# Kernel optimization log

Hardware: AMD Instinct MI355X
Metric: run time of the kernel (lower is better)

The kernel has to match this reference:

```python
import jax, jax.numpy as jnp
import numpy as np

B, F, E = 1024, 1024, 256      # batch, flat_shape (mobilenet), embedding_size
L1, L2, L3 = 16, 8, 32         # level1 classes, level2 classes per branch, level3 classes per leaf
NE3 = L1 * L2                  # 128 leaf (level-3) classifier heads


def setup_inputs() -> dict:
    key = jax.random.key(0)
    ks = jax.random.split(key, 10)
    w = lambda k, shape: (jax.random.normal(k, shape, jnp.float32) * 0.02)
    return {
        "features_x": jax.random.normal(ks[0], (B, F), jnp.float32),
        "features_y": jax.random.normal(ks[1], (B, F), jnp.float32),
        # level-1 head: Linear(F->E, no bias) + LayerNorm + ReLU + Linear(E->L1)
        "l1_W1": w(ks[2], (F, E)),
        "l1_g": jnp.ones((E,), jnp.float32), "l1_b": jnp.zeros((E,), jnp.float32),
        "l1_W2": w(ks[3], (E, L1)), "l1_b2": jnp.zeros((L1,), jnp.float32),
        # level-2 heads (one per level-1 class), stacked on a leading expert axis
        "l2_W1": w(ks[4], (L1, F, E)),
        "l2_g": jnp.ones((L1, E), jnp.float32), "l2_b": jnp.zeros((L1, E), jnp.float32),
        "l2_W2": w(ks[5], (L1, E, L2)), "l2_b2": jnp.zeros((L1, L2), jnp.float32),
        # level-3 heads (flattened [level1][level2] -> NE3 experts)
        "l3_W1": w(ks[6], (NE3, F, E)),
        "l3_g": jnp.ones((NE3, E), jnp.float32), "l3_b": jnp.zeros((NE3, E), jnp.float32),
        "l3_W2": w(ks[7], (NE3, E, L3)), "l3_b2": jnp.zeros((NE3, L3), jnp.float32),
    }


def _ln(h, g, b, eps=1e-5):
    m = jnp.mean(h, axis=-1, keepdims=True)
    v = jnp.mean(jnp.square(h - m), axis=-1, keepdims=True)
    return (h - m) * jax.lax.rsqrt(v + eps) * g + b


def reference(features_x, features_y,
              l1_W1, l1_g, l1_b, l1_W2, l1_b2,
              l2_W1, l2_g, l2_b, l2_W2, l2_b2,
              l3_W1, l3_g, l3_b, l3_W2, l3_b2):
    # Dropout is identity in eval mode.
    x, y = features_x, features_y
    rows = jnp.arange(x.shape[0])

    # level 1: single head on x
    h1 = jax.nn.relu(_ln(x @ l1_W1, l1_g, l1_b))
    logits1 = h1 @ l1_W2 + l1_b2                                # [B, L1]
    idx1 = jnp.argmax(logits1, axis=-1)                         # argmax(softmax) == argmax

    # level 2: routed head on 0.6*x + 0.4*y; compute all L1 heads batched, gather selected
    ft = 0.6 * x + 0.4 * y
    h2 = jax.nn.relu(_ln(jnp.einsum('bf,efh->beh', ft, l2_W1), l2_g, l2_b))  # [B, L1, E]
    logits2_all = jnp.einsum('beh,ehc->bec', h2, l2_W2) + l2_b2              # [B, L1, L2]
    logits2 = logits2_all[rows, idx1]                                        # [B, L2]
    idx2 = jnp.argmax(logits2, axis=-1)

    # level 3: doubly-routed head on x; flat expert index = idx1*L2 + idx2
    eidx = idx1 * logits2.shape[-1] + idx2
    h3 = jax.nn.relu(_ln(jnp.einsum('bf,efh->beh', x, l3_W1), l3_g, l3_b))   # [B, NE3, E]
    logits3_all = jnp.einsum('beh,ehc->bec', h3, l3_W2) + l3_b2              # [B, NE3, L3]
    logits3 = logits3_all[rows, eidx]                                        # [B, L3]

    # uniform class counts => pad_sequence is a no-op
    return (logits1, logits2, logits3)
```

## Files before the change

### kernel.cpp

```cpp
#include <hip/hip_runtime.h>


#define B_    1024
#define F_    1024
#define E_    256
#define NL1   16
#define NL2   8
#define NL3   32
#define NE3_  128
#define CS1   4
#define CS2   8
#define CS3   16
#define MAXCH2 160
#define MAXCH3 192
#define OUT2_OFF (B_ * NL1)
#define OUT3_OFF (B_ * (NL1 + NL2))

typedef __attribute__((ext_vector_type(8))) short bf16x8_t;
typedef __attribute__((ext_vector_type(4))) float f32x4_t;

__device__ __forceinline__ float b2f(unsigned short u) {
    union { unsigned int i; float f; } v; v.i = ((unsigned int)u) << 16; return v.f;
}
__device__ __forceinline__ unsigned short f2b(float f) {
    union { float f; unsigned int i; } v; v.f = f;
    unsigned int x = v.i; x += 0x7fffu + ((x >> 16) & 1u);
    return (unsigned short)(x >> 16);
}

template<int R, int NC>
__device__ void head_chunk(
    const float* __restrict__ in,
    const void* W1v, const void* gv_, const void* bv_,
    const void* W2v, const void* b2v, int bf,
    float* part, float* hn, float* red, float* lg, int t)
{
    const int lane = t & 63;
    const int grp  = t >> 6;
    const int e0   = lane * 4;

    float acc[R][4];
    #pragma unroll
    for (int r = 0; r < R; ++r) { acc[r][0]=0.f; acc[r][1]=0.f; acc[r][2]=0.f; acc[r][3]=0.f; }

    const float* ing = in + grp * 256;

    if (bf) {
        const unsigned short* W = (const unsigned short*)W1v + (size_t)grp * 256 * E_;
        for (int f0 = 0; f0 < 256; f0 += 16) {
            ushort4 w[16];
            #pragma unroll
            for (int k = 0; k < 16; ++k)
                w[k] = *(const ushort4*)(W + (size_t)(f0 + k) * E_ + e0);
            #pragma unroll
            for (int q = 0; q < 4; ++q) {
                float4 xq[R];
                #pragma unroll
                for (int r = 0; r < R; ++r)
                    xq[r] = *(const float4*)(ing + r * F_ + f0 + q * 4);
                #pragma unroll
                for (int k2 = 0; k2 < 4; ++k2) {
                    ushort4 ww = w[q * 4 + k2];
                    float w0 = b2f(ww.x), w1 = b2f(ww.y), w2 = b2f(ww.z), w3 = b2f(ww.w);
                    #pragma unroll
                    for (int r = 0; r < R; ++r) {
                        float xv = (k2 == 0) ? xq[r].x : (k2 == 1) ? xq[r].y
                                 : (k2 == 2) ? xq[r].z : xq[r].w;
                        acc[r][0] += xv * w0; acc[r][1] += xv * w1;
                        acc[r][2] += xv * w2; acc[r][3] += xv * w3;
                    }
                }
            }
        }
    } else {
        const float* W = (const float*)W1v + (size_t)grp * 256 * E_;
        for (int f0 = 0; f0 < 256; f0 += 8) {
            float4 w[8];
            #pragma unroll
            for (int k = 0; k < 8; ++k)
                w[k] = *(const float4*)(W + (size_t)(f0 + k) * E_ + e0);
            #pragma unroll
            for (int q = 0; q < 2; ++q) {
                float4 xq[R];
                #pragma unroll
                for (int r = 0; r < R; ++r)
                    xq[r] = *(const float4*)(ing + r * F_ + f0 + q * 4);
                #pragma unroll
                for (int k2 = 0; k2 < 4; ++k2) {
                    float4 ww = w[q * 4 + k2];
                    #pragma unroll
                    for (int r = 0; r < R; ++r) {
                        float xv = (k2 == 0) ? xq[r].x : (k2 == 1) ? xq[r].y
                                 : (k2 == 2) ? xq[r].z : xq[r].w;
                        acc[r][0] += xv * ww.x; acc[r][1] += xv * ww.y;
                        acc[r][2] += xv * ww.z; acc[r][3] += xv * ww.w;
                    }
                }
            }
        }
    }

    #pragma unroll
    for (int r = 0; r < R; ++r) {
        part[(size_t)(grp * R + r) * E_ + e0 + 0] = acc[r][0];
        part[(size_t)(grp * R + r) * E_ + e0 + 1] = acc[r][1];
        part[(size_t)(grp * R + r) * E_ + e0 + 2] = acc[r][2];
        part[(size_t)(grp * R + r) * E_ + e0 + 3] = acc[r][3];
    }
    __syncthreads();

    float h[R];
    #pragma unroll
    for (int r = 0; r < R; ++r)
        h[r] = part[(0 * R + r) * E_ + t] + part[(1 * R + r) * E_ + t]
             + part[(2 * R + r) * E_ + t] + part[(3 * R + r) * E_ + t];

    #pragma unroll
    for (int r = 0; r < R; ++r) {
        float s = h[r], ss = h[r] * h[r];
        #pragma unroll
        for (int o = 32; o > 0; o >>= 1) { s += __shfl_xor(s, o); ss += __shfl_xor(ss, o); }
        if (lane == 0) { red[(grp * R + r) * 2 + 0] = s; red[(grp * R + r) * 2 + 1] = ss; }
    }
    __syncthreads();

    float gv, bv;
    if (bf) { gv = b2f(((const unsigned short*)gv_)[t]); bv = b2f(((const unsigned short*)bv_)[t]); }
    else    { gv = ((const float*)gv_)[t];               bv = ((const float*)bv_)[t]; }

    #pragma unroll
    for (int r = 0; r < R; ++r) {
        float S  = red[(0*R+r)*2] + red[(1*R+r)*2] + red[(2*R+r)*2] + red[(3*R+r)*2];
        float SS = red[(0*R+r)*2+1] + red[(1*R+r)*2+1] + red[(2*R+r)*2+1] + red[(3*R+r)*2+1];
        float m    = S * (1.0f / E_);
        float var  = SS * (1.0f / E_) - m * m;
        float rstd = rsqrtf(var + 1e-5f);
        hn[r * E_ + t] = fmaxf((h[r] - m) * rstd * gv + bv, 0.0f);
    }
    __syncthreads();

    constexpr int RN = R * NC;
    constexpr int G  = 256 / RN;
    constexpr int CH = E_ / G;
    const int oi = t % RN, j = t / RN, r = oi / NC, c = oi % NC;
    float a = 0.f;
    if (bf) {
        const unsigned short* W = (const unsigned short*)W2v;
        #pragma unroll 8
        for (int e = j * CH; e < j * CH + CH; ++e) a += hn[r * E_ + e] * b2f(W[(size_t)e * NC + c]);
    } else {
        const float* W = (const float*)W2v;
        #pragma unroll 8
        for (int e = j * CH; e < j * CH + CH; ++e) a += hn[r * E_ + e] * W[(size_t)e * NC + c];
    }
    float bias = bf ? b2f(((const unsigned short*)b2v)[c]) : ((const float*)b2v)[c];
    if (G > 1) {
        part[t] = a;
        __syncthreads();
        if (j == 0) {
            float sum = a;
            #pragma unroll
            for (int jj = 1; jj < G; ++jj) sum += part[jj * RN + oi];
            lg[oi] = sum + bias;
        }
    } else {
        lg[oi] = a + bias;
    }
    __syncthreads();
}

__global__ void dtype_sniff_kernel(const unsigned int* l1g_words, int* flag) {
    if (threadIdx.x == 0 && blockIdx.x == 0)
        *flag = (l1g_words[0] == 0x3F803F80u) ? 1 : 0;
}

__global__ __launch_bounds__(256) void mlc_level1_kernel(
    const void* x, const void* W1, const void* g, const void* b,
    const void* W2, const void* b2, void* out, int* idx1, const int* flagp)
{
    __shared__ float in_s[CS1 * F_];
    __shared__ float part[4 * CS1 * E_];
    __shared__ float hn[CS1 * E_];
    __shared__ float red[4 * CS1 * 2];
    __shared__ float lg[CS1 * NL1];

    const int t = threadIdx.x;
    const int bf = *flagp;
    const int row0 = blockIdx.x * CS1;

    #pragma unroll
    for (int r = 0; r < CS1; ++r) {
        if (bf) {
            ushort4 xv = ((const ushort4*)x)[(size_t)(row0 + r) * 256 + t];
            in_s[r * F_ + t*4+0] = b2f(xv.x); in_s[r * F_ + t*4+1] = b2f(xv.y);
            in_s[r * F_ + t*4+2] = b2f(xv.z); in_s[r * F_ + t*4+3] = b2f(xv.w);
        } else {
            float4 xv = ((const float4*)x)[(size_t)(row0 + r) * 256 + t];
            in_s[r * F_ + t*4+0] = xv.x; in_s[r * F_ + t*4+1] = xv.y;
            in_s[r * F_ + t*4+2] = xv.z; in_s[r * F_ + t*4+3] = xv.w;
        }
    }
    __syncthreads();

    head_chunk<CS1, NL1>(in_s, W1, g, b, W2, b2, bf, part, hn, red, lg, t);

    if (t < CS1 * NL1) {
        int r = t / NL1, c = t % NL1;
        size_t o = (size_t)(row0 + r) * NL1 + c;
        if (bf) ((unsigned short*)out)[o] = f2b(lg[t]);
        else    ((float*)out)[o] = lg[t];
        if (c == 0) {
            float best = lg[r * NL1]; int bi = 0;
            #pragma unroll
            for (int cc = 1; cc < NL1; ++cc)
                if (lg[r * NL1 + cc] > best) { best = lg[r * NL1 + cc]; bi = cc; }
            idx1[row0 + r] = bi;
        }
    }
}

template<int NEXP, int MAXCH, int CHUNK>
__global__ __launch_bounds__(1024) void mlc_route_kernel(
    const int* __restrict__ src, int* __restrict__ rows_out, int4* __restrict__ chunks_out)
{
    __shared__ int hist[NEXP], offs[NEXP], cur[NEXP];
    const int t = threadIdx.x;
    if (t < NEXP) hist[t] = 0;
    __syncthreads();
    int e = src[t];
    if (e < 0) e = 0; if (e >= NEXP) e = NEXP - 1;
    atomicAdd(&hist[e], 1);
    __syncthreads();
    if (t == 0) {
        int o = 0;
        for (int i = 0; i < NEXP; ++i) { offs[i] = o; cur[i] = o; o += hist[i]; }
    }
    __syncthreads();
    int pos = atomicAdd(&cur[e], 1);
    if (pos >= 0 && pos < B_) rows_out[pos] = t;
    if (t == 0) {
        int nch = 0;
        for (int i = 0; i < NEXP; ++i) {
            int n = hist[i], st = offs[i];
            for (int j = 0; j < n && nch < MAXCH; j += CHUNK)
                chunks_out[nch++] = make_int4(i, st + j, min(CHUNK, n - j), 0);
        }
        for (; nch < MAXCH; ++nch) chunks_out[nch] = make_int4(0, 0, 0, 0);
    }
}

__global__ __launch_bounds__(256) void mlc_level2_kernel(
    const void* x, const void* y,
    const void* W1b, const void* gb, const void* bb,
    const void* W2b, const void* b2b,
    const int4* __restrict__ chunks, const int* __restrict__ rowlist,
    void* out, int* eidx, const int* flagp)
{
    __shared__ float in_s[CS2 * F_];
    __shared__ float part[4 * CS2 * E_];
    __shared__ float hn[CS2 * E_];
    __shared__ float red[4 * CS2 * 2];
    __shared__ float lg[CS2 * NL2];
    __shared__ int4  chs;
    __shared__ int   rows_s[CS2];

    const int t = threadIdx.x;
    const int bf = *flagp;

    if (t == 0) chs = chunks[blockIdx.x];
    __syncthreads();
    const int expert = chs.x, start = chs.y, count = chs.z;
    if (count <= 0) return;
    if (t < CS2) rows_s[t] = (t < count) ? rowlist[start + t] : -1;
    __syncthreads();

    #pragma unroll
    for (int r = 0; r < CS2; ++r) {
        int row = rows_s[r];
        float f0 = 0.f, f1 = 0.f, f2 = 0.f, f3 = 0.f;
        if (row >= 0) {
            if (bf) {
                ushort4 xv = ((const ushort4*)x)[(size_t)row * 256 + t];
                ushort4 yv = ((const ushort4*)y)[(size_t)row * 256 + t];
                f0 = 0.6f * b2f(xv.x) + 0.4f * b2f(yv.x);
                f1 = 0.6f * b2f(xv.y) + 0.4f * b2f(yv.y);
                f2 = 0.6f * b2f(xv.z) + 0.4f * b2f(yv.z);
                f3 = 0.6f * b2f(xv.w) + 0.4f * b2f(yv.w);
            } else {
                float4 xv = ((const float4*)x)[(size_t)row * 256 + t];
                float4 yv = ((const float4*)y)[(size_t)row * 256 + t];
                f0 = 0.6f * xv.x + 0.4f * yv.x; f1 = 0.6f * xv.y + 0.4f * yv.y;
                f2 = 0.6f * xv.z + 0.4f * yv.z; f3 = 0.6f * xv.w + 0.4f * yv.w;
            }
        }
        in_s[r * F_ + t*4+0] = f0; in_s[r * F_ + t*4+1] = f1;
        in_s[r * F_ + t*4+2] = f2; in_s[r * F_ + t*4+3] = f3;
    }
    __syncthreads();

    const void* W1 = bf ? (const void*)((const unsigned short*)W1b + (size_t)expert * F_ * E_)
                        : (const void*)((const float*)W1b + (size_t)expert * F_ * E_);
    const void* g  = bf ? (const void*)((const unsigned short*)gb + (size_t)expert * E_)
                        : (const void*)((const float*)gb + (size_t)expert * E_);
    const void* b  = bf ? (const void*)((const unsigned short*)bb + (size_t)expert * E_)
                        : (const void*)((const float*)bb + (size_t)expert * E_);
    const void* W2 = bf ? (const void*)((const unsigned short*)W2b + (size_t)expert * E_ * NL2)
                        : (const void*)((const float*)W2b + (size_t)expert * E_ * NL2);
    const void* b2 = bf ? (const void*)((const unsigned short*)b2b + (size_t)expert * NL2)
                        : (const void*)((const float*)b2b + (size_t)expert * NL2);

    head_chunk<CS2, NL2>(in_s, W1, g, b, W2, b2, bf, part, hn, red, lg, t);

    if (t < CS2 * NL2) {
        int r = t / NL2, c = t % NL2;
        if (r < count) {
            size_t o = (size_t)OUT2_OFF + (size_t)rows_s[r] * NL2 + c;
            if (bf) ((unsigned short*)out)[o] = f2b(lg[t]);
            else    ((float*)out)[o] = lg[t];
            if (c == 0) {
                float best = lg[r * NL2]; int bi = 0;
                #pragma unroll
                for (int cc = 1; cc < NL2; ++cc)
                    if (lg[r * NL2 + cc] > best) { best = lg[r * NL2 + cc]; bi = cc; }
                eidx[rows_s[r]] = expert * NL2 + bi;
            }
        }
    }
}


__device__ __forceinline__ void stage_rows(
    unsigned short* xs, const void* xg, const int* rows, int bf, int t)
{
    const int r = t >> 4;
    const int row = rows[r];
    #pragma unroll
    for (int i = 0; i < 8; ++i) {
        const int c  = (t & 15) + 16 * i;
        const int cs = c ^ (r & 7);
        uint4 v = make_uint4(0u, 0u, 0u, 0u);
        if (row >= 0) {
            if (bf) {
                v = *(const uint4*)((const unsigned short*)xg + (size_t)row * F_ + c * 8);
            } else {
                const float* xf = (const float*)xg + (size_t)row * F_ + c * 8;
                float4 fa = *(const float4*)xf;
                float4 fb = *(const float4*)(xf + 4);
                v.x = ((unsigned)f2b(fa.y) << 16) | f2b(fa.x);
                v.y = ((unsigned)f2b(fa.w) << 16) | f2b(fa.z);
                v.z = ((unsigned)f2b(fb.y) << 16) | f2b(fb.x);
                v.w = ((unsigned)f2b(fb.w) << 16) | f2b(fb.z);
            }
        }
        *(uint4*)(xs + (size_t)r * F_ + cs * 8) = v;
    }
}

__device__ void mfma_w1s(const unsigned short* xs, const void* W1v, int bf,
                         float* h, int t)
{
    const int l    = t & 63;
    const int w    = t >> 6;
    const int u    = l >> 4;
    const int row  = l & 15;
    const int colb = w * 64 + row;

    f32x4_t acc[4];
    #pragma unroll
    for (int tl = 0; tl < 4; ++tl) acc[tl] = (f32x4_t){0.f, 0.f, 0.f, 0.f};

    if (bf) {
        const unsigned short* __restrict__ W = (const unsigned short*)W1v;
        for (int k0 = 0; k0 < F_; k0 += 32) {
            const int cs = ((k0 >> 3) + u) ^ (row & 7);
            bf16x8_t ax = *(const bf16x8_t*)(xs + (size_t)row * F_ + cs * 8);
            const unsigned short* __restrict__ Wk = W + (size_t)(k0 + u * 8) * E_ + colb;
            #pragma unroll
            for (int tl = 0; tl < 4; ++tl) {
                bf16x8_t b;
                #pragma unroll
                for (int e = 0; e < 8; ++e) b[e] = (short)Wk[e * E_ + tl * 16];
                acc[tl] = __builtin_amdgcn_mfma_f32_16x16x32_bf16(ax, b, acc[tl], 0, 0, 0);
            }
        }
    } else {
        const float* __restrict__ W = (const float*)W1v;
        for (int k0 = 0; k0 < F_; k0 += 32) {
            const int cs = ((k0 >> 3) + u) ^ (row & 7);
            bf16x8_t ax = *(const bf16x8_t*)(xs + (size_t)row * F_ + cs * 8);
            const float* __restrict__ Wk = W + (size_t)(k0 + u * 8) * E_ + colb;
            #pragma unroll
            for (int tl = 0; tl < 4; ++tl) {
                bf16x8_t b;
                #pragma unroll
                for (int e = 0; e < 8; ++e) b[e] = (short)f2b(Wk[e * E_ + tl * 16]);
                acc[tl] = __builtin_amdgcn_mfma_f32_16x16x32_bf16(ax, b, acc[tl], 0, 0, 0);
            }
        }
    }

    #pragma unroll
    for (int tl = 0; tl < 4; ++tl) {
        #pragma unroll
        for (int j = 0; j < 4; ++j)
            h[(size_t)(u * 4 + j) * E_ + colb + tl * 16] = acc[tl][j];
    }
}

__device__ void ln_relu16(float* h, const void* g_, const void* b_,
                          int bf, int t, float* red)
{
    __syncthreads();
    const int l = t & 63, w = t >> 6;
    float hv[16];
    #pragma unroll
    for (int r = 0; r < 16; ++r) hv[r] = h[(size_t)r * E_ + t];

    #pragma unroll
    for (int r = 0; r < 16; ++r) {
        float s = hv[r], ss = hv[r] * hv[r];
        #pragma unroll
        for (int o = 32; o > 0; o >>= 1) { s += __shfl_xor(s, o); ss += __shfl_xor(ss, o); }
        if (l == 0) { red[(w * 16 + r) * 2] = s; red[(w * 16 + r) * 2 + 1] = ss; }
    }
    __syncthreads();

    float gv, bv;
    if (bf) { gv = b2f(((const unsigned short*)g_)[t]); bv = b2f(((const unsigned short*)b_)[t]); }
    else    { gv = ((const float*)g_)[t];               bv = ((const float*)b_)[t]; }

    #pragma unroll
    for (int r = 0; r < 16; ++r) {
        float S  = red[r * 2]     + red[(16 + r) * 2]     + red[(32 + r) * 2]     + red[(48 + r) * 2];
        float SS = red[r * 2 + 1] + red[(16 + r) * 2 + 1] + red[(32 + r) * 2 + 1] + red[(48 + r) * 2 + 1];
        float m    = S * (1.0f / E_);
        float var  = SS * (1.0f / E_) - m * m;
        float rstd = rsqrtf(var + 1e-5f);
        h[(size_t)r * E_ + t] = fmaxf((hv[r] - m) * rstd * gv + bv, 0.0f);
    }
    __syncthreads();
}

__global__ __launch_bounds__(256) void MultiLevelClassifier_26491358282059_kernel(
    const void* x,
    const void* W1b, const void* gb, const void* bb,
    const void* W2b, const void* b2b,
    const int4* __restrict__ chunks, const int* __restrict__ rowlist,
    void* out, const int* flagp)
{
    __shared__ __align__(16) unsigned short xs[16 * F_];
    __shared__ float h[16 * E_];
    __shared__ float red[128];
    __shared__ int4  chs;
    __shared__ int   rows_s[16];

    const int t  = threadIdx.x;
    const int bf = *flagp;

    if (t == 0) chs = chunks[blockIdx.x];
    __syncthreads();
    const int expert = chs.x, start = chs.y, count = chs.z;
    if (count <= 0) return;
    if (t < 16) rows_s[t] = (t < count) ? rowlist[start + t] : -1;
    __syncthreads();

    stage_rows(xs, x, rows_s, bf, t);
    __syncthreads();

    const void* W1 = bf ? (const void*)((const unsigned short*)W1b + (size_t)expert * F_ * E_)
                        : (const void*)((const float*)W1b + (size_t)expert * F_ * E_);
    const void* g  = bf ? (const void*)((const unsigned short*)gb + (size_t)expert * E_)
                        : (const void*)((const float*)gb + (size_t)expert * E_);
    const void* b  = bf ? (const void*)((const unsigned short*)bb + (size_t)expert * E_)
                        : (const void*)((const float*)bb + (size_t)expert * E_);
    const void* W2 = bf ? (const void*)((const unsigned short*)W2b + (size_t)expert * E_ * NL3)
                        : (const void*)((const float*)W2b + (size_t)expert * E_ * NL3);
    const void* b2 = bf ? (const void*)((const unsigned short*)b2b + (size_t)expert * NL3)
                        : (const void*)((const float*)b2b + (size_t)expert * NL3);

    mfma_w1s(xs, W1, bf, h, t);
    ln_relu16(h, g, b, bf, t, red);

    {
        const int r = t >> 4, c0 = t & 15;
        float a0 = 0.f, a1 = 0.f;
        if (bf) {
            const unsigned short* W = (const unsigned short*)W2;
            #pragma unroll 4
            for (int e = 0; e < E_; ++e) {
                float hv = h[(size_t)r * E_ + e];
                a0 += hv * b2f(W[(size_t)e * NL3 + c0]);
                a1 += hv * b2f(W[(size_t)e * NL3 + c0 + 16]);
            }
        } else {
            const float* W = (const float*)W2;
            #pragma unroll 4
            for (int e = 0; e < E_; ++e) {
                float hv = h[(size_t)r * E_ + e];
                a0 += hv * W[(size_t)e * NL3 + c0];
                a1 += hv * W[(size_t)e * NL3 + c0 + 16];
            }
        }
        if (r < count) {
            float bb0, bb1;
            if (bf) { bb0 = b2f(((const unsigned short*)b2)[c0]); bb1 = b2f(((const unsigned short*)b2)[c0 + 16]); }
            else    { bb0 = ((const float*)b2)[c0];               bb1 = ((const float*)b2)[c0 + 16]; }
            size_t o = (size_t)OUT3_OFF + (size_t)rows_s[r] * NL3 + c0;
            if (bf) {
                ((unsigned short*)out)[o]      = f2b(a0 + bb0);
                ((unsigned short*)out)[o + 16] = f2b(a1 + bb1);
            } else {
                ((float*)out)[o]      = a0 + bb0;
                ((float*)out)[o + 16] = a1 + bb1;
            }
        }
    }
}

extern "C" void kernel_launch(void* const* d_in, const int* in_sizes, int n_in,
                              void* d_out, int out_size, void* d_ws, size_t ws_size,
                              hipStream_t stream) {
    (void)in_sizes; (void)n_in; (void)out_size; (void)ws_size;

    int* ws = (int*)d_ws;
    int*  flag  = ws;
    int*  idx1  = ws + 64;
    int*  eidx  = ws + 1088;
    int*  rows2 = ws + 2112;
    int*  rows3 = ws + 3136;
    int4* ch2   = (int4*)(ws + 4160);
    int4* ch3   = (int4*)(ws + 4800);

    dtype_sniff_kernel<<<1, 1, 0, stream>>>((const unsigned int*)d_in[3], flag);

    mlc_level1_kernel<<<B_ / CS1, 256, 0, stream>>>(
        d_in[0], d_in[2], d_in[3], d_in[4], d_in[5], d_in[6],
        d_out, idx1, flag);

    mlc_route_kernel<NL1, MAXCH2, CS2><<<1, 1024, 0, stream>>>(idx1, rows2, ch2);

    mlc_level2_kernel<<<MAXCH2, 256, 0, stream>>>(
        d_in[0], d_in[1], d_in[7], d_in[8], d_in[9], d_in[10], d_in[11],
        ch2, rows2, d_out, eidx, flag);

    mlc_route_kernel<NE3_, MAXCH3, CS3><<<1, 1024, 0, stream>>>(eidx, rows3, ch3);

    MultiLevelClassifier_26491358282059_kernel<<<MAXCH3, 256, 0, stream>>>(
        d_in[0], d_in[12], d_in[13], d_in[14], d_in[15], d_in[16],
        ch3, rows3, d_out, flag);
}
```

Before: 360.6 us.

## Split level-3 GEMM over K across blocks and parallelize routing scans

The level-3 expert GEMM is split into four K-slices, each computed by its own block into a workspace buffer. A second kernel sums the slices and applies LayerNorm, ReLU and the output projection, with two blocks per chunk. The routing kernel replaces its serial single-thread prefix sums and chunk emission with a parallel scan. Level-1 and level-2 chunk sizes are halved for more blocks, and padded LayerNorm rows avoid shared-memory bank conflicts. In exchange it adds an extra launch and a round trip of partial sums through global memory, and it falls back to the old single-kernel path when the workspace is too small.

```diff
diff --git a/kernel.cpp b/kernel.cpp
--- a/kernel.cpp
+++ b/kernel.cpp
@@ -8,13 +8,17 @@
 #define NL2   8
 #define NL3   32
 #define NE3_  128
-#define CS1   4
-#define CS2   8
+#define CS1   2
+#define CS2   4
 #define CS3   16
-#define MAXCH2 160
+#define KS3   4
+#define MAXCH2 272
 #define MAXCH3 192
 #define OUT2_OFF (B_ * NL1)
 #define OUT3_OFF (B_ * (NL1 + NL2))
+#define H4_BYTE_OFF 65536
+#define H4_BYTES   ((size_t)MAXCH3 * KS3 * 16 * E_ * 4)
+#define HNS (E_ + 4)
 
 typedef __attribute__((ext_vector_type(8))) short bf16x8_t;
 typedef __attribute__((ext_vector_type(4))) float f32x4_t;
@@ -135,36 +139,33 @@
         float m    = S * (1.0f / E_);
         float var  = SS * (1.0f / E_) - m * m;
         float rstd = rsqrtf(var + 1e-5f);
-        hn[r * E_ + t] = fmaxf((h[r] - m) * rstd * gv + bv, 0.0f);
+        hn[r * HNS + t] = fmaxf((h[r] - m) * rstd * gv + bv, 0.0f);
     }
     __syncthreads();
 
     constexpr int RN = R * NC;
-    constexpr int G  = 256 / RN;
+    constexpr int G  = 4;
     constexpr int CH = E_ / G;
-    const int oi = t % RN, j = t / RN, r = oi / NC, c = oi % NC;
     float a = 0.f;
-    if (bf) {
-        const unsigned short* W = (const unsigned short*)W2v;
-        #pragma unroll 8
-        for (int e = j * CH; e < j * CH + CH; ++e) a += hn[r * E_ + e] * b2f(W[(size_t)e * NC + c]);
-    } else {
-        const float* W = (const float*)W2v;
-        #pragma unroll 8
-        for (int e = j * CH; e < j * CH + CH; ++e) a += hn[r * E_ + e] * W[(size_t)e * NC + c];
-    }
-    float bias = bf ? b2f(((const unsigned short*)b2v)[c]) : ((const float*)b2v)[c];
-    if (G > 1) {
-        part[t] = a;
-        __syncthreads();
-        if (j == 0) {
-            float sum = a;
-            #pragma unroll
-            for (int jj = 1; jj < G; ++jj) sum += part[jj * RN + oi];
-            lg[oi] = sum + bias;
-        }
-    } else {
-        lg[oi] = a + bias;
+    if (t < RN * G) {
+        const int oi = t % RN, j = t / RN, r = oi / NC, c = oi % NC;
+        if (bf) {
+            const unsigned short* W = (const unsigned short*)W2v;
+            #pragma unroll 8
+            for (int e = j * CH; e < j * CH + CH; ++e) a += hn[r * HNS + e] * b2f(W[(size_t)e * NC + c]);
+        } else {
+            const float* W = (const float*)W2v;
+            #pragma unroll 8
+            for (int e = j * CH; e < j * CH + CH; ++e) a += hn[r * HNS + e] * W[(size_t)e * NC + c];
+        }
+    }
+    part[t] = a;
+    __syncthreads();
+    if (t < RN) {
+        const int c = t % NC;
+        float sum = part[t] + part[RN + t] + part[2 * RN + t] + part[3 * RN + t];
+        float bias = bf ? b2f(((const unsigned short*)b2v)[c]) : ((const float*)b2v)[c];
+        lg[t] = sum + bias;
     }
     __syncthreads();
 }
@@ -180,7 +181,7 @@
 {
     __shared__ float in_s[CS1 * F_];
     __shared__ float part[4 * CS1 * E_];
-    __shared__ float hn[CS1 * E_];
+    __shared__ float hn[CS1 * HNS];
     __shared__ float red[4 * CS1 * 2];
     __shared__ float lg[CS1 * NL1];
 
@@ -223,7 +224,8 @@
 __global__ __launch_bounds__(1024) void mlc_route_kernel(
     const int* __restrict__ src, int* __restrict__ rows_out, int4* __restrict__ chunks_out)
 {
-    __shared__ int hist[NEXP], offs[NEXP], cur[NEXP];
+    __shared__ int hist[NEXP], offs[NEXP], cur[NEXP], cOff[NEXP];
+    __shared__ int sA[NEXP], sB[NEXP];
     const int t = threadIdx.x;
     if (t < NEXP) hist[t] = 0;
     __syncthreads();
@@ -231,22 +233,30 @@
     if (e < 0) e = 0; if (e >= NEXP) e = NEXP - 1;
     atomicAdd(&hist[e], 1);
     __syncthreads();
-    if (t == 0) {
-        int o = 0;
-        for (int i = 0; i < NEXP; ++i) { offs[i] = o; cur[i] = o; o += hist[i]; }
+    if (t < NEXP) { sA[t] = hist[t]; sB[t] = (hist[t] + CHUNK - 1) / CHUNK; }
+    __syncthreads();
+    for (int d = 1; d < NEXP; d <<= 1) {
+        int va = 0, vb = 0;
+        if (t < NEXP && t >= d) { va = sA[t - d]; vb = sB[t - d]; }
+        __syncthreads();
+        if (t < NEXP) { sA[t] += va; sB[t] += vb; }
+        __syncthreads();
+    }
+    if (t < NEXP) {
+        int ex = sA[t] - hist[t];
+        offs[t] = ex; cur[t] = ex;
+        cOff[t] = sB[t] - (hist[t] + CHUNK - 1) / CHUNK;
     }
     __syncthreads();
     int pos = atomicAdd(&cur[e], 1);
     if (pos >= 0 && pos < B_) rows_out[pos] = t;
-    if (t == 0) {
-        int nch = 0;
-        for (int i = 0; i < NEXP; ++i) {
-            int n = hist[i], st = offs[i];
-            for (int j = 0; j < n && nch < MAXCH; j += CHUNK)
-                chunks_out[nch++] = make_int4(i, st + j, min(CHUNK, n - j), 0);
-        }
-        for (; nch < MAXCH; ++nch) chunks_out[nch] = make_int4(0, 0, 0, 0);
-    }
+    const int ctot = sB[NEXP - 1];
+    if (t < NEXP) {
+        int n = hist[t], st = offs[t], c0 = cOff[t], k = 0;
+        for (int j = 0; j < n; j += CHUNK, ++k)
+            chunks_out[c0 + k] = make_int4(t, st + j, min(CHUNK, n - j), 0);
+    }
+    for (int s = ctot + t; s < MAXCH; s += 1024) chunks_out[s] = make_int4(0, 0, 0, 0);
 }
 
 __global__ __launch_bounds__(256) void mlc_level2_kernel(
@@ -258,7 +268,7 @@
 {
     __shared__ float in_s[CS2 * F_];
     __shared__ float part[4 * CS2 * E_];
-    __shared__ float hn[CS2 * E_];
+    __shared__ float hn[CS2 * HNS];
     __shared__ float red[4 * CS2 * 2];
     __shared__ float lg[CS2 * NL2];
     __shared__ int4  chs;
@@ -329,7 +339,190 @@
 }
 
 
-__device__ __forceinline__ void stage_rows(
+__global__ __launch_bounds__(256) void mlc_l3_partial_kernel(
+    const void* x, const void* W1b,
+    const int4* __restrict__ chunks, const int* __restrict__ rowlist,
+    float* __restrict__ h4, const int* flagp)
+{
+    __shared__ __align__(16) unsigned short xs[16 * 256];
+    __shared__ int4 chs;
+    __shared__ int  rows_s[16];
+
+    const int t  = threadIdx.x;
+    const int bf = *flagp;
+    const int c  = blockIdx.x >> 2;
+    const int ks = blockIdx.x & 3;
+
+    if (t == 0) chs = chunks[c];
+    __syncthreads();
+    const int expert = chs.x, start = chs.y, count = chs.z;
+    if (count <= 0) return;
+    if (t < 16) rows_s[t] = (t < count) ? rowlist[start + t] : -1;
+    __syncthreads();
+
+    {
+        const int r = t >> 4;
+        const int row = rows_s[r];
+        #pragma unroll
+        for (int i = 0; i < 2; ++i) {
+            const int c2 = (t & 15) + 16 * i;
+            const int cs = c2 ^ (r & 7);
+            uint4 v = make_uint4(0u, 0u, 0u, 0u);
+            if (row >= 0) {
+                if (bf) {
+                    v = *(const uint4*)((const unsigned short*)x + (size_t)row * F_ + ks * 256 + c2 * 8);
+                } else {
+                    const float* xf = (const float*)x + (size_t)row * F_ + ks * 256 + c2 * 8;
+                    float4 fa = *(const float4*)xf;
+                    float4 fb = *(const float4*)(xf + 4);
+                    v.x = ((unsigned)f2b(fa.y) << 16) | f2b(fa.x);
+                    v.y = ((unsigned)f2b(fa.w) << 16) | f2b(fa.z);
+                    v.z = ((unsigned)f2b(fb.y) << 16) | f2b(fb.x);
+                    v.w = ((unsigned)f2b(fb.w) << 16) | f2b(fb.z);
+                }
+            }
+            *(uint4*)(xs + r * 256 + cs * 8) = v;
+        }
+    }
+    __syncthreads();
+
+    const int l    = t & 63;
+    const int w    = t >> 6;
+    const int u    = l >> 4;
+    const int row  = l & 15;
+    const int colb = w * 64 + row;
+
+    f32x4_t acc[4];
+    #pragma unroll
+    for (int tl = 0; tl < 4; ++tl) acc[tl] = (f32x4_t){0.f, 0.f, 0.f, 0.f};
+
+    if (bf) {
+        const unsigned short* __restrict__ W =
+            (const unsigned short*)W1b + (size_t)expert * F_ * E_ + (size_t)ks * 256 * E_;
+        #pragma unroll 2
+        for (int k0 = 0; k0 < 256; k0 += 32) {
+            const int cs = ((k0 >> 3) + u) ^ (row & 7);
+            bf16x8_t ax = *(const bf16x8_t*)(xs + row * 256 + cs * 8);
+            const unsigned short* __restrict__ Wk = W + (size_t)(k0 + u * 8) * E_ + colb;
+            #pragma unroll
+            for (int tl = 0; tl < 4; ++tl) {
+                bf16x8_t b;
+                #pragma unroll
+                for (int e = 0; e < 8; ++e) b[e] = (short)Wk[e * E_ + tl * 16];
+                acc[tl] = __builtin_amdgcn_mfma_f32_16x16x32_bf16(ax, b, acc[tl], 0, 0, 0);
+            }
+        }
+    } else {
+        const float* __restrict__ W =
+            (const float*)W1b + (size_t)expert * F_ * E_ + (size_t)ks * 256 * E_;
+        #pragma unroll 2
+        for (int k0 = 0; k0 < 256; k0 += 32) {
+            const int cs = ((k0 >> 3) + u) ^ (row & 7);
+            bf16x8_t ax = *(const bf16x8_t*)(xs + row * 256 + cs * 8);
+            const float* __restrict__ Wk = W + (size_t)(k0 + u * 8) * E_ + colb;
+            #pragma unroll
+            for (int tl = 0; tl < 4; ++tl) {
+                bf16x8_t b;
+                #pragma unroll
+                for (int e = 0; e < 8; ++e) b[e] = (short)f2b(Wk[e * E_ + tl * 16]);
+                acc[tl] = __builtin_amdgcn_mfma_f32_16x16x32_bf16(ax, b, acc[tl], 0, 0, 0);
+            }
+        }
+    }
+
+    float* hd = h4 + (size_t)(c * KS3 + ks) * 16 * E_;
+    #pragma unroll
+    for (int tl = 0; tl < 4; ++tl) {
+        #pragma unroll
+        for (int j = 0; j < 4; ++j)
+            hd[(size_t)(u * 4 + j) * E_ + colb + tl * 16] = acc[tl][j];
+    }
+}
+
+__global__ __launch_bounds__(256) void MultiLevelClassifier_26491358282059_kernel(
+    const void* gb, const void* bb, const void* W2b, const void* b2b,
+    const int4* __restrict__ chunks, const int* __restrict__ rowlist,
+    const float* __restrict__ h4, void* out, const int* flagp)
+{
+    __shared__ float hn[8 * HNS];
+    __shared__ float red[4 * 8 * 2];
+    __shared__ int4  chs;
+    __shared__ int   rows_s[16];
+
+    const int t    = threadIdx.x;
+    const int bf   = *flagp;
+    const int c    = blockIdx.x >> 1;
+    const int half = blockIdx.x & 1;
+
+    if (t == 0) chs = chunks[c];
+    __syncthreads();
+    const int expert = chs.x, start = chs.y, count = chs.z;
+    if (count <= 0) return;
+    if (t < 16) rows_s[t] = (t < count) ? rowlist[start + t] : -1;
+    __syncthreads();
+
+    const int l = t & 63, w = t >> 6;
+
+    float hv[8];
+    #pragma unroll
+    for (int m = 0; m < 8; ++m) {
+        const float* p = h4 + (size_t)(c * KS3) * 16 * E_ + (size_t)(half * 8 + m) * E_ + t;
+        hv[m] = p[0] + p[16 * E_] + p[32 * E_] + p[48 * E_];
+    }
+
+    #pragma unroll
+    for (int m = 0; m < 8; ++m) {
+        float s = hv[m], ss = hv[m] * hv[m];
+        #pragma unroll
+        for (int o = 32; o > 0; o >>= 1) { s += __shfl_xor(s, o); ss += __shfl_xor(ss, o); }
+        if (l == 0) { red[(w * 8 + m) * 2] = s; red[(w * 8 + m) * 2 + 1] = ss; }
+    }
+    __syncthreads();
+
+    float gv, bv;
+    if (bf) {
+        gv = b2f(((const unsigned short*)gb)[(size_t)expert * E_ + t]);
+        bv = b2f(((const unsigned short*)bb)[(size_t)expert * E_ + t]);
+    } else {
+        gv = ((const float*)gb)[(size_t)expert * E_ + t];
+        bv = ((const float*)bb)[(size_t)expert * E_ + t];
+    }
+
+    #pragma unroll
+    for (int m = 0; m < 8; ++m) {
+        float S  = red[m * 2]     + red[(8 + m) * 2]     + red[(16 + m) * 2]     + red[(24 + m) * 2];
+        float SS = red[m * 2 + 1] + red[(8 + m) * 2 + 1] + red[(16 + m) * 2 + 1] + red[(24 + m) * 2 + 1];
+        float mean = S * (1.0f / E_);
+        float var  = SS * (1.0f / E_) - mean * mean;
+        float rstd = rsqrtf(var + 1e-5f);
+        hn[m * HNS + t] = fmaxf((hv[m] - mean) * rstd * gv + bv, 0.0f);
+    }
+    __syncthreads();
+
+    {
+        const int r = t >> 5, c0 = t & 31;
+        float a = 0.f;
+        if (bf) {
+            const unsigned short* W = (const unsigned short*)W2b + (size_t)expert * E_ * NL3;
+            #pragma unroll 8
+            for (int e = 0; e < E_; ++e) a += hn[r * HNS + e] * b2f(W[(size_t)e * NL3 + c0]);
+        } else {
+            const float* W = (const float*)W2b + (size_t)expert * E_ * NL3;
+            #pragma unroll 8
+            for (int e = 0; e < E_; ++e) a += hn[r * HNS + e] * W[(size_t)e * NL3 + c0];
+        }
+        const int rr = half * 8 + r;
+        if (rr < count) {
+            float bias = bf ? b2f(((const unsigned short*)b2b)[(size_t)expert * NL3 + c0])
+                            : ((const float*)b2b)[(size_t)expert * NL3 + c0];
+            size_t o = (size_t)OUT3_OFF + (size_t)rows_s[rr] * NL3 + c0;
+            if (bf) ((unsigned short*)out)[o] = f2b(a + bias);
+            else    ((float*)out)[o] = a + bias;
+        }
+    }
+}
+
+__device__ __forceinline__ void stage_rows_full(
     unsigned short* xs, const void* xg, const int* rows, int bf, int t)
 {
     const int r = t >> 4;
@@ -356,92 +549,7 @@
     }
 }
 
-__device__ void mfma_w1s(const unsigned short* xs, const void* W1v, int bf,
-                         float* h, int t)
-{
-    const int l    = t & 63;
-    const int w    = t >> 6;
-    const int u    = l >> 4;
-    const int row  = l & 15;
-    const int colb = w * 64 + row;
-
-    f32x4_t acc[4];
-    #pragma unroll
-    for (int tl = 0; tl < 4; ++tl) acc[tl] = (f32x4_t){0.f, 0.f, 0.f, 0.f};
-
-    if (bf) {
-        const unsigned short* __restrict__ W = (const unsigned short*)W1v;
-        for (int k0 = 0; k0 < F_; k0 += 32) {
-            const int cs = ((k0 >> 3) + u) ^ (row & 7);
-            bf16x8_t ax = *(const bf16x8_t*)(xs + (size_t)row * F_ + cs * 8);
-            const unsigned short* __restrict__ Wk = W + (size_t)(k0 + u * 8) * E_ + colb;
-            #pragma unroll
-            for (int tl = 0; tl < 4; ++tl) {
-                bf16x8_t b;
-                #pragma unroll
-                for (int e = 0; e < 8; ++e) b[e] = (short)Wk[e * E_ + tl * 16];
-                acc[tl] = __builtin_amdgcn_mfma_f32_16x16x32_bf16(ax, b, acc[tl], 0, 0, 0);
-            }
-        }
-    } else {
-        const float* __restrict__ W = (const float*)W1v;
-        for (int k0 = 0; k0 < F_; k0 += 32) {
-            const int cs = ((k0 >> 3) + u) ^ (row & 7);
-            bf16x8_t ax = *(const bf16x8_t*)(xs + (size_t)row * F_ + cs * 8);
-            const float* __restrict__ Wk = W + (size_t)(k0 + u * 8) * E_ + colb;
-            #pragma unroll
-            for (int tl = 0; tl < 4; ++tl) {
-                bf16x8_t b;
-                #pragma unroll
-                for (int e = 0; e < 8; ++e) b[e] = (short)f2b(Wk[e * E_ + tl * 16]);
-                acc[tl] = __builtin_amdgcn_mfma_f32_16x16x32_bf16(ax, b, acc[tl], 0, 0, 0);
-            }
-        }
-    }
-
-    #pragma unroll
-    for (int tl = 0; tl < 4; ++tl) {
-        #pragma unroll
-        for (int j = 0; j < 4; ++j)
-            h[(size_t)(u * 4 + j) * E_ + colb + tl * 16] = acc[tl][j];
-    }
-}
-
-__device__ void ln_relu16(float* h, const void* g_, const void* b_,
-                          int bf, int t, float* red)
-{
-    __syncthreads();
-    const int l = t & 63, w = t >> 6;
-    float hv[16];
-    #pragma unroll
-    for (int r = 0; r < 16; ++r) hv[r] = h[(size_t)r * E_ + t];
-
-    #pragma unroll
-    for (int r = 0; r < 16; ++r) {
-        float s = hv[r], ss = hv[r] * hv[r];
-        #pragma unroll
-        for (int o = 32; o > 0; o >>= 1) { s += __shfl_xor(s, o); ss += __shfl_xor(ss, o); }
-        if (l == 0) { red[(w * 16 + r) * 2] = s; red[(w * 16 + r) * 2 + 1] = ss; }
-    }
-    __syncthreads();
-
-    float gv, bv;
-    if (bf) { gv = b2f(((const unsigned short*)g_)[t]); bv = b2f(((const unsigned short*)b_)[t]); }
-    else    { gv = ((const float*)g_)[t];               bv = ((const float*)b_)[t]; }
-
-    #pragma unroll
-    for (int r = 0; r < 16; ++r) {
-        float S  = red[r * 2]     + red[(16 + r) * 2]     + red[(32 + r) * 2]     + red[(48 + r) * 2];
-        float SS = red[r * 2 + 1] + red[(16 + r) * 2 + 1] + red[(32 + r) * 2 + 1] + red[(48 + r) * 2 + 1];
-        float m    = S * (1.0f / E_);
-        float var  = SS * (1.0f / E_) - m * m;
-        float rstd = rsqrtf(var + 1e-5f);
-        h[(size_t)r * E_ + t] = fmaxf((hv[r] - m) * rstd * gv + bv, 0.0f);
-    }
-    __syncthreads();
-}
-
-__global__ __launch_bounds__(256) void MultiLevelClassifier_26491358282059_kernel(
+__global__ __launch_bounds__(256) void mlc_level3_mono_kernel(
     const void* x,
     const void* W1b, const void* gb, const void* bb,
     const void* W2b, const void* b2b,
@@ -464,47 +572,105 @@
     if (t < 16) rows_s[t] = (t < count) ? rowlist[start + t] : -1;
     __syncthreads();
 
-    stage_rows(xs, x, rows_s, bf, t);
-    __syncthreads();
-
-    const void* W1 = bf ? (const void*)((const unsigned short*)W1b + (size_t)expert * F_ * E_)
-                        : (const void*)((const float*)W1b + (size_t)expert * F_ * E_);
-    const void* g  = bf ? (const void*)((const unsigned short*)gb + (size_t)expert * E_)
-                        : (const void*)((const float*)gb + (size_t)expert * E_);
-    const void* b  = bf ? (const void*)((const unsigned short*)bb + (size_t)expert * E_)
-                        : (const void*)((const float*)bb + (size_t)expert * E_);
-    const void* W2 = bf ? (const void*)((const unsigned short*)W2b + (size_t)expert * E_ * NL3)
-                        : (const void*)((const float*)W2b + (size_t)expert * E_ * NL3);
-    const void* b2 = bf ? (const void*)((const unsigned short*)b2b + (size_t)expert * NL3)
-                        : (const void*)((const float*)b2b + (size_t)expert * NL3);
-
-    mfma_w1s(xs, W1, bf, h, t);
-    ln_relu16(h, g, b, bf, t, red);
+    stage_rows_full(xs, x, rows_s, bf, t);
+    __syncthreads();
+
+    const int l = t & 63, w = t >> 6, u = l >> 4, row = l & 15;
+    const int colb = w * 64 + row;
+    f32x4_t acc[4];
+    #pragma unroll
+    for (int tl = 0; tl < 4; ++tl) acc[tl] = (f32x4_t){0.f, 0.f, 0.f, 0.f};
+
+    if (bf) {
+        const unsigned short* __restrict__ W = (const unsigned short*)W1b + (size_t)expert * F_ * E_;
+        for (int k0 = 0; k0 < F_; k0 += 32) {
+            const int cs = ((k0 >> 3) + u) ^ (row & 7);
+            bf16x8_t ax = *(const bf16x8_t*)(xs + (size_t)row * F_ + cs * 8);
+            const unsigned short* __restrict__ Wk = W + (size_t)(k0 + u * 8) * E_ + colb;
+            #pragma unroll
+            for (int tl = 0; tl < 4; ++tl) {
+                bf16x8_t b;
+                #pragma unroll
+                for (int e = 0; e < 8; ++e) b[e] = (short)Wk[e * E_ + tl * 16];
+                acc[tl] = __builtin_amdgcn_mfma_f32_16x16x32_bf16(ax, b, acc[tl], 0, 0, 0);
+            }
+        }
+    } else {
+        const float* __restrict__ W = (const float*)W1b + (size_t)expert * F_ * E_;
+        for (int k0 = 0; k0 < F_; k0 += 32) {
+            const int cs = ((k0 >> 3) + u) ^ (row & 7);
+            bf16x8_t ax = *(const bf16x8_t*)(xs + (size_t)row * F_ + cs * 8);
+            const float* __restrict__ Wk = W + (size_t)(k0 + u * 8) * E_ + colb;
+            #pragma unroll
+            for (int tl = 0; tl < 4; ++tl) {
+                bf16x8_t b;
+                #pragma unroll
+                for (int e = 0; e < 8; ++e) b[e] = (short)f2b(Wk[e * E_ + tl * 16]);
+                acc[tl] = __builtin_amdgcn_mfma_f32_16x16x32_bf16(ax, b, acc[tl], 0, 0, 0);
+            }
+        }
+    }
+    #pragma unroll
+    for (int tl = 0; tl < 4; ++tl) {
+        #pragma unroll
+        for (int j = 0; j < 4; ++j)
+            h[(size_t)(u * 4 + j) * E_ + colb + tl * 16] = acc[tl][j];
+    }
+    __syncthreads();
+
+    float hv[16];
+    #pragma unroll
+    for (int r = 0; r < 16; ++r) hv[r] = h[(size_t)r * E_ + t];
+    #pragma unroll
+    for (int r = 0; r < 16; ++r) {
+        float s = hv[r], ss = hv[r] * hv[r];
+        #pragma unroll
+        for (int o = 32; o > 0; o >>= 1) { s += __shfl_xor(s, o); ss += __shfl_xor(ss, o); }
+        if (l == 0) { red[(w * 16 + r) * 2] = s; red[(w * 16 + r) * 2 + 1] = ss; }
+    }
+    __syncthreads();
+    float gv, bv;
+    if (bf) { gv = b2f(((const unsigned short*)gb)[(size_t)expert * E_ + t]);
+              bv = b2f(((const unsigned short*)bb)[(size_t)expert * E_ + t]); }
+    else    { gv = ((const float*)gb)[(size_t)expert * E_ + t];
+              bv = ((const float*)bb)[(size_t)expert * E_ + t]; }
+    #pragma unroll
+    for (int r = 0; r < 16; ++r) {
+        float S  = red[r * 2]     + red[(16 + r) * 2]     + red[(32 + r) * 2]     + red[(48 + r) * 2];
+        float SS = red[r * 2 + 1] + red[(16 + r) * 2 + 1] + red[(32 + r) * 2 + 1] + red[(48 + r) * 2 + 1];
+        float mean = S * (1.0f / E_);
+        float var  = SS * (1.0f / E_) - mean * mean;
+        float rstd = rsqrtf(var + 1e-5f);
+        h[(size_t)r * E_ + t] = fmaxf((hv[r] - mean) * rstd * gv + bv, 0.0f);
+    }
+    __syncthreads();
 
     {
         const int r = t >> 4, c0 = t & 15;
         float a0 = 0.f, a1 = 0.f;
         if (bf) {
-            const unsigned short* W = (const unsigned short*)W2;
+            const unsigned short* W = (const unsigned short*)W2b + (size_t)expert * E_ * NL3;
             #pragma unroll 4
             for (int e = 0; e < E_; ++e) {
-                float hv = h[(size_t)r * E_ + e];
-                a0 += hv * b2f(W[(size_t)e * NL3 + c0]);
-                a1 += hv * b2f(W[(size_t)e * NL3 + c0 + 16]);
+                float hh = h[(size_t)r * E_ + e];
+                a0 += hh * b2f(W[(size_t)e * NL3 + c0]);
+                a1 += hh * b2f(W[(size_t)e * NL3 + c0 + 16]);
             }
         } else {
-            const float* W = (const float*)W2;
+            const float* W = (const float*)W2b + (size_t)expert * E_ * NL3;
             #pragma unroll 4
             for (int e = 0; e < E_; ++e) {
-                float hv = h[(size_t)r * E_ + e];
-                a0 += hv * W[(size_t)e * NL3 + c0];
-                a1 += hv * W[(size_t)e * NL3 + c0 + 16];
+                float hh = h[(size_t)r * E_ + e];
+                a0 += hh * W[(size_t)e * NL3 + c0];
+                a1 += hh * W[(size_t)e * NL3 + c0 + 16];
             }
         }
         if (r < count) {
             float bb0, bb1;
-            if (bf) { bb0 = b2f(((const unsigned short*)b2)[c0]); bb1 = b2f(((const unsigned short*)b2)[c0 + 16]); }
-            else    { bb0 = ((const float*)b2)[c0];               bb1 = ((const float*)b2)[c0 + 16]; }
+            if (bf) { bb0 = b2f(((const unsigned short*)b2b)[(size_t)expert * NL3 + c0]);
+                      bb1 = b2f(((const unsigned short*)b2b)[(size_t)expert * NL3 + c0 + 16]); }
+            else    { bb0 = ((const float*)b2b)[(size_t)expert * NL3 + c0];
+                      bb1 = ((const float*)b2b)[(size_t)expert * NL3 + c0 + 16]; }
             size_t o = (size_t)OUT3_OFF + (size_t)rows_s[r] * NL3 + c0;
             if (bf) {
                 ((unsigned short*)out)[o]      = f2b(a0 + bb0);
@@ -520,7 +686,7 @@
 extern "C" void kernel_launch(void* const* d_in, const int* in_sizes, int n_in,
                               void* d_out, int out_size, void* d_ws, size_t ws_size,
                               hipStream_t stream) {
-    (void)in_sizes; (void)n_in; (void)out_size; (void)ws_size;
+    (void)in_sizes; (void)n_in; (void)out_size;
 
     int* ws = (int*)d_ws;
     int*  flag  = ws;
@@ -529,7 +695,10 @@
     int*  rows2 = ws + 2112;
     int*  rows3 = ws + 3136;
     int4* ch2   = (int4*)(ws + 4160);
-    int4* ch3   = (int4*)(ws + 4800);
+    int4* ch3   = (int4*)(ws + 5248);
+    float* h4   = (float*)((char*)d_ws + H4_BYTE_OFF);
+
+    const bool big_ws = ws_size >= (size_t)H4_BYTE_OFF + H4_BYTES;
 
     dtype_sniff_kernel<<<1, 1, 0, stream>>>((const unsigned int*)d_in[3], flag);
 
@@ -545,7 +714,15 @@
 
     mlc_route_kernel<NE3_, MAXCH3, CS3><<<1, 1024, 0, stream>>>(eidx, rows3, ch3);
 
-    MultiLevelClassifier_26491358282059_kernel<<<MAXCH3, 256, 0, stream>>>(
-        d_in[0], d_in[12], d_in[13], d_in[14], d_in[15], d_in[16],
-        ch3, rows3, d_out, flag);
-}
+    if (big_ws) {
+        mlc_l3_partial_kernel<<<MAXCH3 * KS3, 256, 0, stream>>>(
+            d_in[0], d_in[12], ch3, rows3, h4, flag);
+        MultiLevelClassifier_26491358282059_kernel<<<MAXCH3 * 2, 256, 0, stream>>>(
+            d_in[13], d_in[14], d_in[15], d_in[16],
+            ch3, rows3, h4, d_out, flag);
+    } else {
+        mlc_level3_mono_kernel<<<MAXCH3, 256, 0, stream>>>(
+            d_in[0], d_in[12], d_in[13], d_in[14], d_in[15], d_in[16],
+            ch3, rows3, d_out, flag);
+    }
+}
```

After: 329.1 us. -8.7%, faster.
